# Performance work log

Hardware: AMD Instinct MI355X
Metric: run time of the kernel (lower is better)

## Reference

```python
import jax, jax.numpy as jnp
import numpy as np

EPS = 1e-12  # torch F.normalize eps


def setup_inputs() -> dict:
    key = jax.random.key(0)
    k1, k2, k3 = jax.random.split(key, 3)
    B, way, shot, D, H, W = 64, 5, 1, 640, 5, 5
    nq = 75
    base = jax.random.normal(k1, (B, way, shot, D, H, W), dtype=jnp.float32)
    query = jax.random.normal(k2, (B, nq, D, H, W), dtype=jnp.float32)
    r = jax.random.normal(k3, (2,), dtype=jnp.float32) * 0.1
    return {"base": base, "query": query, "r": r, "neighbor_k": 5}


def reference(base, query, r, neighbor_k):
    B, way, shot, D, H, W = base.shape
    nq = query.shape[1]
    hw = H * W

    # ---- global-cosine branch: spatial-mean descriptors ----
    base_mean = base.reshape(B, way * shot, D, hw).mean(axis=-1)   # [B, way*shot, D]
    query_mean = query.reshape(B, nq, D, hw).mean(axis=-1)         # [B, nq, D]
    bm = base_mean / jnp.maximum(jnp.linalg.norm(base_mean, axis=-1, keepdims=True), EPS)
    qm = query_mean / jnp.maximum(jnp.linalg.norm(query_mean, axis=-1, keepdims=True), EPS)
    logits = jnp.einsum('bqd,bkd->bqk', qm, bm)                    # [B, nq, way*shot]

    # ---- DN4 image-to-class branch (vectorized over the original triple loop) ----
    # query local descriptors: [B, nq, hw, D], L2-normalized over channels
    q = query.reshape(B, nq, D, hw).transpose(0, 1, 3, 2)
    q = q / jnp.linalg.norm(q, axis=-1, keepdims=True)
    # support local descriptors: base_mix [B, way, shot*D, hw], column-normalized
    s = base.reshape(B, way, shot * D, hw)
    s = s / jnp.linalg.norm(s, axis=2, keepdims=True)
    # cosine sims between every query patch and every support patch of each class
    # (requires shot*D == D, i.e. shot == 1, as in the original code)
    sim = jnp.einsum('bqpd,bkdl->bqkpl', q, s)                     # [B, nq, way, hw, hw]
    topk_vals, _ = jax.lax.top_k(sim, neighbor_k)                  # [B, nq, way, hw, k]
    logits_dn4 = topk_vals.sum(axis=(-1, -2)) / neighbor_k         # [B, nq, way]

    return r[0] * logits + r[1] * logits_dn4
```

## Files before the change

### kernel.cpp

```cpp
#include <hip/hip_runtime.h>
#include <hip/hip_bf16.h>
#include <math.h>

#define NB    64
#define WAY   5
#define DCH   640
#define HW    25
#define NQ    75
#define NBK   5
#define EPSN  1e-12f

#define QPB   4
#define BPB   ((NQ + QPB - 1) / QPB)
#define NDG   (DCH / 8)
#define SCOLS 128

typedef __attribute__((ext_vector_type(8)))  short  bf16x8;
typedef __attribute__((ext_vector_type(8)))  ushort u16x8;
typedef __attribute__((ext_vector_type(16))) float  f32x16;
typedef __attribute__((ext_vector_type(4)))  float  f32x4;

__device__ inline ushort f2bf(float f) {
    uint u = __float_as_uint(f);
    return (ushort)((u + 0x7FFFu + ((u >> 16) & 1u)) >> 16);
}

__global__ __launch_bounds__(256) void k_prep(const float* __restrict__ base,
                                              float* __restrict__ invs,
                                              float* __restrict__ invsm,
                                              ushort* __restrict__ sT)
{
    const int bk = blockIdx.x;
    const int b  = bk / WAY;
    const int k  = bk - b * WAY;
    const float* src = base + (size_t)bk * (DCH * HW);
    __shared__ float lds[DCH * HW];
    __shared__ float red[256];
    const int tid = threadIdx.x;

    const f32x4* s4 = (const f32x4*)src;
    f32x4* l4 = (f32x4*)lds;
    for (int i = tid; i < (DCH * HW) / 4; i += 256)
        l4[i] = __builtin_nontemporal_load(s4 + i);
    __syncthreads();

    if (tid < HW) {
        float ss = 0.f;
        for (int d = 0; d < DCH; ++d) { float v = lds[d * HW + tid]; ss = fmaf(v, v, ss); }
        invs[bk * HW + tid] = rsqrtf(ss);
    }

    float ssq = 0.f;
    for (int d = tid; d < DCH; d += 256) {
        float s = 0.f;
        #pragma unroll
        for (int pp = 0; pp < HW; ++pp) s += lds[d * HW + pp];
        float m = s * (1.0f / HW);
        ssq = fmaf(m, m, ssq);
    }
    red[tid] = ssq;
    __syncthreads();
    for (int s = 128; s > 0; s >>= 1) {
        if (tid < s) red[tid] += red[tid + s];
        __syncthreads();
    }
    if (tid == 0) invsm[bk] = 1.0f / fmaxf(sqrtf(red[0]), EPSN);

    ushort* dstb = sT + (size_t)b * (NDG * SCOLS * 8);
    for (int t = tid; t < NDG * HW; t += 256) {
        const int dg = t / HW, l = t - dg * HW;
        u16x8 v;
        #pragma unroll
        for (int e = 0; e < 8; ++e) v[e] = f2bf(lds[(dg * 8 + e) * HW + l]);
        *(u16x8*)&dstb[((size_t)dg * SCOLS + k * HW + l) * 8] = v;
    }
    if (k == 0) {
        const u16x8 z = (u16x8)(ushort)0;
        for (int t = tid; t < NDG * 3; t += 256) {
            const int dg = t / 3, sc = 125 + (t - dg * 3);
            *(u16x8*)&dstb[((size_t)dg * SCOLS + sc) * 8] = z;
        }
    }
}

__global__ __launch_bounds__(256, 3) void k_fused(const float* __restrict__ query,
                                                  const ushort* __restrict__ sT,
                                                  const float* __restrict__ invs,
                                                  const float* __restrict__ invsm,
                                                  const float* __restrict__ r,
                                                  float* __restrict__ out)
{
    __shared__ float invs_l[WAY * HW];
    __shared__ float invsm_l[WAY];

    const int tid  = threadIdx.x;
    const int wid  = tid >> 6;
    const int lane = tid & 63;
    const int p    = lane & 31;
    const int hi   = lane >> 5;

    const int wk = (blockIdx.x & 7) * (int)(gridDim.x >> 3) + (blockIdx.x >> 3);
    const int b  = wk / BPB;
    const int qb = wk - b * BPB;
    const int q  = qb * QPB + wid;
    const bool qok = q < NQ;

    if (tid < WAY * HW) invs_l[tid] = invs[b * WAY * HW + tid];
    if (tid < WAY)      invsm_l[tid] = invsm[b * WAY + tid];
    __syncthreads();
    if (!qok) return;

    f32x16 acc0 = {}, acc1 = {}, acc2 = {}, acc3 = {}, accg = {};
    float ssq = 0.f;

    const int pc = (p < HW) ? p : (HW - 1);
    const float* qp = query + (size_t)(b * NQ + q) * (DCH * HW) + pc;
    const ushort* sTb = sT + (size_t)b * (NDG * SCOLS * 8);

    #pragma unroll 4
    for (int st = 0; st < DCH / 16; ++st) {
        const int dg = st * 2 + hi;
        const float* qs = qp + (size_t)(st * 16 + hi * 8) * HW;
        bf16x8 bq;
        #pragma unroll
        for (int e = 0; e < 8; ++e) {
            const float v = __builtin_nontemporal_load(qs + e * HW);
            ssq = fmaf(v, v, ssq);
            bq[e] = (short)f2bf(v);
        }
        const bf16x8* arow = (const bf16x8*)(sTb + (size_t)dg * SCOLS * 8);
        const bf16x8 a0 = arow[p];
        const bf16x8 a1 = arow[32 + p];
        const bf16x8 a2 = arow[64 + p];
        const bf16x8 a3 = arow[96 + p];
        acc0 = __builtin_amdgcn_mfma_f32_32x32x16_bf16(a0, bq, acc0, 0, 0, 0);
        acc1 = __builtin_amdgcn_mfma_f32_32x32x16_bf16(a1, bq, acc1, 0, 0, 0);
        acc2 = __builtin_amdgcn_mfma_f32_32x32x16_bf16(a2, bq, acc2, 0, 0, 0);
        acc3 = __builtin_amdgcn_mfma_f32_32x32x16_bf16(a3, bq, acc3, 0, 0, 0);
        accg = __builtin_amdgcn_mfma_f32_32x32x16_bf16(bq, bq, accg, 0, 0, 0);
    }

    const bool pok = p < HW;

    ssq += __shfl_xor(ssq, 32);
    const float invq = rsqrtf(ssq);

    float gs[WAY] = {0.f, 0.f, 0.f, 0.f, 0.f};
    float qq = 0.f;
    #pragma unroll
    for (int rr = 0; rr < 16; ++rr) {
        const int rowb = (rr & 3) + 8 * (rr >> 2);
        const float v0 = hi ? 0.f : accg[rr];
        const float v1 = hi ? accg[rr] : 0.f;
        if (rowb < HW)     qq += v0;
        if (rowb + 4 < HW) qq += v1;
    }
#define TILE_SUM(ACC, T)                                            \
    _Pragma("unroll")                                               \
    for (int rr = 0; rr < 16; ++rr) {                               \
        const int s0 = (T) * 32 + (rr & 3) + 8 * (rr >> 2);         \
        const float v0 = hi ? 0.f : ACC[rr];                        \
        const float v1 = hi ? ACC[rr] : 0.f;                        \
        if (s0 < 125)     gs[s0 / 25]       += v0;                  \
        if (s0 + 4 < 125) gs[(s0 + 4) / 25] += v1;                  \
    }
    TILE_SUM(acc0, 0) TILE_SUM(acc1, 1) TILE_SUM(acc2, 2) TILE_SUM(acc3, 3)
#undef TILE_SUM

    if (!pok) {
        qq = 0.f;
        #pragma unroll
        for (int g = 0; g < WAY; ++g) gs[g] = 0.f;
    }
    #pragma unroll
    for (int o = 1; o < 64; o <<= 1) {
        qq += __shfl_xor(qq, o);
        #pragma unroll
        for (int g = 0; g < WAY; ++g) gs[g] += __shfl_xor(gs[g], o);
    }

    float A[64];
    #pragma unroll
    for (int rr = 0; rr < 16; ++rr) {
        A[rr] = acc0[rr]; A[16 + rr] = acc1[rr]; A[32 + rr] = acc2[rr]; A[48 + rr] = acc3[rr];
    }

    float tots[WAY];
    #pragma unroll
    for (int g = 0; g < WAY; ++g) {
        float v[HW];
        #pragma unroll
        for (int j = 0; j < HW; ++j) {
            const int scol = g * HW + j;
            const int t = scol >> 5, row = scol & 31;
            const int hreq = (row >> 2) & 1;
            const int rr = (row & 3) | ((row >> 3) << 2);
            float mine = (hi == hreq) ? A[t * 16 + rr] : 0.f;
            mine += __shfl_xor(mine, 32);
            v[j] = mine * invq * invs_l[scol];
        }
        float gtot = 0.f;
        #pragma unroll
        for (int it = 0; it < NBK; ++it) {
            float m = v[0];
            #pragma unroll
            for (int j = 1; j < HW; ++j) m = fmaxf(m, v[j]);
            gtot += m;
            bool rem = false;
            #pragma unroll
            for (int j = 0; j < HW; ++j) {
                const bool hit = (!rem) && (v[j] == m);
                v[j] = hit ? -3.402823466e38f : v[j];
                rem = rem || hit;
            }
        }
        tots[g] = pok ? gtot : 0.f;
    }
    #pragma unroll
    for (int o = 1; o < 64; o <<= 1) {
        #pragma unroll
        for (int g = 0; g < WAY; ++g) tots[g] += __shfl_xor(tots[g], o);
    }

    const float r0 = r[0], r1 = r[1];
    const float invqm = 1.0f / fmaxf(sqrtf(qq) * (1.0f / HW), EPSN);
    float res[WAY];
    #pragma unroll
    for (int g = 0; g < WAY; ++g)
        res[g] = r0 * gs[g] * (1.0f / 625.0f) * invqm * invsm_l[g]
               + r1 * tots[g] * 0.5f * (1.0f / NBK);

    float ov = res[0];
    ov = (lane == 1) ? res[1] : ov;
    ov = (lane == 2) ? res[2] : ov;
    ov = (lane == 3) ? res[3] : ov;
    ov = (lane == 4) ? res[4] : ov;
    if (lane < WAY) out[(size_t)(b * NQ + q) * WAY + lane] = ov;
}

extern "C" void kernel_launch(void* const* d_in, const int* in_sizes, int n_in,
                              void* d_out, int out_size, void* d_ws, size_t ws_size,
                              hipStream_t stream)
{
    const float* base  = (const float*)d_in[0];
    const float* query = (const float*)d_in[1];
    const float* r     = (const float*)d_in[2];
    float* out = (float*)d_out;

    float* invs   = (float*)d_ws;
    float* invsm  = invs + NB * WAY * HW;
    ushort* sT    = (ushort*)((float*)d_ws + 16384);

    k_prep<<<NB * WAY, 256, 0, stream>>>(base, invs, invsm, sT);
    k_fused<<<NB * BPB, 256, 0, stream>>>(query, sT, invs, invsm, r, out);
}
```

Before: 134.2 us.

## Stage query chunks through double-buffered LDS with coalesced vector loads

Replaces the strided per-element nontemporal global loads of the query (stride HW floats per lane) with coalesced float4 loads of contiguous 64-channel chunks into a per-wave double-buffered LDS region. The next chunk is loaded into registers while MFMAs run on the current one, then written to LDS. The aim is to cut uncoalesced global traffic and hide load latency. It adds about 51 KB of LDS per block, which may reduce occupancy below the launch-bounds target of 3 blocks, and it relies on per-wave buffers without explicit barriers.

```diff
diff --git a/kernel.cpp b/kernel.cpp
--- a/kernel.cpp
+++ b/kernel.cpp
@@ -14,6 +14,9 @@
 #define BPB   ((NQ + QPB - 1) / QPB)
 #define NDG   (DCH / 8)
 #define SCOLS 128
+#define CD    64
+#define NCHK  (DCH / CD)
+#define CFL   (CD * HW)
 
 typedef __attribute__((ext_vector_type(8)))  short  bf16x8;
 typedef __attribute__((ext_vector_type(8)))  ushort u16x8;
@@ -90,6 +93,7 @@
                                                   const float* __restrict__ r,
                                                   float* __restrict__ out)
 {
+    __shared__ __align__(16) float lds_q[QPB][2][CFL];
     __shared__ float invs_l[WAY * HW];
     __shared__ float invsm_l[WAY];
 
@@ -114,31 +118,63 @@
     float ssq = 0.f;
 
     const int pc = (p < HW) ? p : (HW - 1);
-    const float* qp = query + (size_t)(b * NQ + q) * (DCH * HW) + pc;
+    const float* qrow = query + (size_t)(b * NQ + q) * (DCH * HW);
     const ushort* sTb = sT + (size_t)b * (NDG * SCOLS * 8);
 
-    #pragma unroll 4
-    for (int st = 0; st < DCH / 16; ++st) {
-        const int dg = st * 2 + hi;
-        const float* qs = qp + (size_t)(st * 16 + hi * 8) * HW;
-        bf16x8 bq;
-        #pragma unroll
-        for (int e = 0; e < 8; ++e) {
-            const float v = __builtin_nontemporal_load(qs + e * HW);
-            ssq = fmaf(v, v, ssq);
-            bq[e] = (short)f2bf(v);
-        }
-        const bf16x8* arow = (const bf16x8*)(sTb + (size_t)dg * SCOLS * 8);
-        const bf16x8 a0 = arow[p];
-        const bf16x8 a1 = arow[32 + p];
-        const bf16x8 a2 = arow[64 + p];
-        const bf16x8 a3 = arow[96 + p];
-        acc0 = __builtin_amdgcn_mfma_f32_32x32x16_bf16(a0, bq, acc0, 0, 0, 0);
-        acc1 = __builtin_amdgcn_mfma_f32_32x32x16_bf16(a1, bq, acc1, 0, 0, 0);
-        acc2 = __builtin_amdgcn_mfma_f32_32x32x16_bf16(a2, bq, acc2, 0, 0, 0);
-        acc3 = __builtin_amdgcn_mfma_f32_32x32x16_bf16(a3, bq, acc3, 0, 0, 0);
-        accg = __builtin_amdgcn_mfma_f32_32x32x16_bf16(bq, bq, accg, 0, 0, 0);
-    }
+    f32x4 ld[7];
+
+#define LOADC(c)                                                              \
+    {                                                                         \
+        const float* src_ = qrow + (c) * CFL;                                 \
+        _Pragma("unroll")                                                     \
+        for (int i = 0; i < 6; ++i)                                           \
+            ld[i] = __builtin_nontemporal_load((const f32x4*)(src_) + i * 64 + lane); \
+        if (lane < 16)                                                        \
+            ld[6] = __builtin_nontemporal_load((const f32x4*)(src_) + 384 + lane); \
+    }
+
+#define WRITEC(buf)                                                           \
+    {                                                                         \
+        f32x4* dst_ = (f32x4*)&lds_q[wid][(buf)][0];                          \
+        _Pragma("unroll")                                                     \
+        for (int i = 0; i < 6; ++i) dst_[i * 64 + lane] = ld[i];              \
+        if (lane < 16) dst_[384 + lane] = ld[6];                              \
+    }
+
+    LOADC(0)
+    WRITEC(0)
+
+    for (int c = 0; c < NCHK; ++c) {
+        const int cur = c & 1;
+        if (c + 1 < NCHK) LOADC(c + 1)
+
+        const float* qb_lds = &lds_q[wid][cur][hi * 8 * HW + pc];
+        #pragma unroll
+        for (int ks = 0; ks < CD / 16; ++ks) {
+            const int dg = c * 8 + ks * 2 + hi;
+            bf16x8 bq;
+            #pragma unroll
+            for (int e = 0; e < 8; ++e) {
+                const float v = qb_lds[(ks * 16 + e) * HW];
+                ssq = fmaf(v, v, ssq);
+                bq[e] = (short)f2bf(v);
+            }
+            const bf16x8* arow = (const bf16x8*)(sTb + (size_t)dg * SCOLS * 8);
+            const bf16x8 a0 = arow[p];
+            const bf16x8 a1 = arow[32 + p];
+            const bf16x8 a2 = arow[64 + p];
+            const bf16x8 a3 = arow[96 + p];
+            acc0 = __builtin_amdgcn_mfma_f32_32x32x16_bf16(a0, bq, acc0, 0, 0, 0);
+            acc1 = __builtin_amdgcn_mfma_f32_32x32x16_bf16(a1, bq, acc1, 0, 0, 0);
+            acc2 = __builtin_amdgcn_mfma_f32_32x32x16_bf16(a2, bq, acc2, 0, 0, 0);
+            acc3 = __builtin_amdgcn_mfma_f32_32x32x16_bf16(a3, bq, acc3, 0, 0, 0);
+            accg = __builtin_amdgcn_mfma_f32_32x32x16_bf16(bq, bq, accg, 0, 0, 0);
+        }
+
+        if (c + 1 < NCHK) WRITEC((c + 1) & 1)
+    }
+#undef LOADC
+#undef WRITEC
 
     const bool pok = p < HW;
 
```

After: 130.5 us. -2.7%, faster.

## Stage query chunks through LDS with async double-buffered loads and streaming top-k

Applied to the files above, without the earlier changes.

Replaces strided per-lane global loads of the query with asynchronous global_load_lds copies of contiguous 64-channel chunks into a per-wave double buffer in LDS. The next chunk's copy is overlapped with the MFMA work on the current one. The epilogue now pre-scales the accumulators by the support norms and replaces the repeated max-and-remove top-5 with a streaming 5-slot insertion network, dropping the 64-float staging array. This adds about 50 KB of LDS per block, which may reduce occupancy, and it depends on hand-placed waitcnt ordering being correct.

```diff
diff --git a/kernel.cpp b/kernel.cpp
--- a/kernel.cpp
+++ b/kernel.cpp
@@ -14,6 +14,9 @@
 #define BPB   ((NQ + QPB - 1) / QPB)
 #define NDG   (DCH / 8)
 #define SCOLS 128
+#define CD    64
+#define NCHK  (DCH / CD)
+#define CFL   (CD * HW)
 
 typedef __attribute__((ext_vector_type(8)))  short  bf16x8;
 typedef __attribute__((ext_vector_type(8)))  ushort u16x8;
@@ -90,7 +93,8 @@
                                                   const float* __restrict__ r,
                                                   float* __restrict__ out)
 {
-    __shared__ float invs_l[WAY * HW];
+    __shared__ __align__(16) float lds_q[QPB][2][CFL];
+    __shared__ float invs_l[SCOLS];
     __shared__ float invsm_l[WAY];
 
     const int tid  = threadIdx.x;
@@ -106,6 +110,7 @@
     const bool qok = q < NQ;
 
     if (tid < WAY * HW) invs_l[tid] = invs[b * WAY * HW + tid];
+    if (tid >= WAY * HW && tid < SCOLS) invs_l[tid] = 0.f;
     if (tid < WAY)      invsm_l[tid] = invsm[b * WAY + tid];
     __syncthreads();
     if (!qok) return;
@@ -114,31 +119,60 @@
     float ssq = 0.f;
 
     const int pc = (p < HW) ? p : (HW - 1);
-    const float* qp = query + (size_t)(b * NQ + q) * (DCH * HW) + pc;
+    const float* qrow = query + (size_t)(b * NQ + q) * (DCH * HW);
     const ushort* sTb = sT + (size_t)b * (NDG * SCOLS * 8);
 
-    #pragma unroll 4
-    for (int st = 0; st < DCH / 16; ++st) {
-        const int dg = st * 2 + hi;
-        const float* qs = qp + (size_t)(st * 16 + hi * 8) * HW;
-        bf16x8 bq;
-        #pragma unroll
-        for (int e = 0; e < 8; ++e) {
-            const float v = __builtin_nontemporal_load(qs + e * HW);
-            ssq = fmaf(v, v, ssq);
-            bq[e] = (short)f2bf(v);
-        }
-        const bf16x8* arow = (const bf16x8*)(sTb + (size_t)dg * SCOLS * 8);
-        const bf16x8 a0 = arow[p];
-        const bf16x8 a1 = arow[32 + p];
-        const bf16x8 a2 = arow[64 + p];
-        const bf16x8 a3 = arow[96 + p];
-        acc0 = __builtin_amdgcn_mfma_f32_32x32x16_bf16(a0, bq, acc0, 0, 0, 0);
-        acc1 = __builtin_amdgcn_mfma_f32_32x32x16_bf16(a1, bq, acc1, 0, 0, 0);
-        acc2 = __builtin_amdgcn_mfma_f32_32x32x16_bf16(a2, bq, acc2, 0, 0, 0);
-        acc3 = __builtin_amdgcn_mfma_f32_32x32x16_bf16(a3, bq, acc3, 0, 0, 0);
-        accg = __builtin_amdgcn_mfma_f32_32x32x16_bf16(bq, bq, accg, 0, 0, 0);
-    }
+#define ISSUE(c)                                                               \
+    {                                                                          \
+        const float* src_ = qrow + (c) * CFL;                                  \
+        float* dst_ = &lds_q[wid][(c) & 1][0];                                 \
+        _Pragma("unroll")                                                      \
+        for (int i = 0; i < 6; ++i)                                            \
+            __builtin_amdgcn_global_load_lds(                                  \
+                (const __attribute__((address_space(1))) uint*)(src_ + i * 256 + lane * 4), \
+                (__attribute__((address_space(3))) uint*)(dst_ + i * 256), 16, 0, 0); \
+        if (lane < 16)                                                         \
+            __builtin_amdgcn_global_load_lds(                                  \
+                (const __attribute__((address_space(1))) uint*)(src_ + 1536 + lane * 4), \
+                (__attribute__((address_space(3))) uint*)(dst_ + 1536), 16, 0, 0); \
+    }
+
+    ISSUE(0)
+
+    for (int c = 0; c < NCHK; ++c) {
+        if (c + 1 < NCHK) {
+            asm volatile("s_waitcnt lgkmcnt(0)" ::: "memory");
+            ISSUE(c + 1)
+            asm volatile("s_waitcnt vmcnt(7)" ::: "memory");
+        } else {
+            asm volatile("s_waitcnt vmcnt(0)" ::: "memory");
+        }
+        __builtin_amdgcn_sched_barrier(0);
+
+        const float* qb_lds = &lds_q[wid][c & 1][hi * 8 * HW + pc];
+        #pragma unroll
+        for (int ks = 0; ks < CD / 16; ++ks) {
+            const int dg = c * 8 + ks * 2 + hi;
+            bf16x8 bq;
+            #pragma unroll
+            for (int e = 0; e < 8; ++e) {
+                const float v = qb_lds[(ks * 16 + e) * HW];
+                ssq = fmaf(v, v, ssq);
+                bq[e] = (short)f2bf(v);
+            }
+            const bf16x8* arow = (const bf16x8*)(sTb + (size_t)dg * SCOLS * 8);
+            const bf16x8 a0 = arow[p];
+            const bf16x8 a1 = arow[32 + p];
+            const bf16x8 a2 = arow[64 + p];
+            const bf16x8 a3 = arow[96 + p];
+            acc0 = __builtin_amdgcn_mfma_f32_32x32x16_bf16(a0, bq, acc0, 0, 0, 0);
+            acc1 = __builtin_amdgcn_mfma_f32_32x32x16_bf16(a1, bq, acc1, 0, 0, 0);
+            acc2 = __builtin_amdgcn_mfma_f32_32x32x16_bf16(a2, bq, acc2, 0, 0, 0);
+            acc3 = __builtin_amdgcn_mfma_f32_32x32x16_bf16(a3, bq, acc3, 0, 0, 0);
+            accg = __builtin_amdgcn_mfma_f32_32x32x16_bf16(bq, bq, accg, 0, 0, 0);
+        }
+    }
+#undef ISSUE
 
     const bool pok = p < HW;
 
@@ -179,42 +213,37 @@
         for (int g = 0; g < WAY; ++g) gs[g] += __shfl_xor(gs[g], o);
     }
 
-    float A[64];
-    #pragma unroll
-    for (int rr = 0; rr < 16; ++rr) {
-        A[rr] = acc0[rr]; A[16 + rr] = acc1[rr]; A[32 + rr] = acc2[rr]; A[48 + rr] = acc3[rr];
-    }
+#define SCALE(ACC, T)                                               \
+    _Pragma("unroll")                                               \
+    for (int rr = 0; rr < 16; ++rr) {                               \
+        const int s0 = (T) * 32 + (rr & 3) + 8 * (rr >> 2);         \
+        ACC[rr] *= invs_l[s0 + 4 * hi];                             \
+    }
+    SCALE(acc0, 0) SCALE(acc1, 1) SCALE(acc2, 2) SCALE(acc3, 3)
+#undef SCALE
 
     float tots[WAY];
     #pragma unroll
     for (int g = 0; g < WAY; ++g) {
-        float v[HW];
+        float t0 = -3.402823466e38f, t1 = t0, t2 = t0, t3 = t0, t4 = t0;
         #pragma unroll
         for (int j = 0; j < HW; ++j) {
             const int scol = g * HW + j;
             const int t = scol >> 5, row = scol & 31;
             const int hreq = (row >> 2) & 1;
             const int rr = (row & 3) | ((row >> 3) << 2);
-            float mine = (hi == hreq) ? A[t * 16 + rr] : 0.f;
+            const float av = (t == 0) ? acc0[rr] : (t == 1) ? acc1[rr]
+                           : (t == 2) ? acc2[rr] : acc3[rr];
+            float mine = (hi == hreq) ? av : 0.f;
             mine += __shfl_xor(mine, 32);
-            v[j] = mine * invq * invs_l[scol];
-        }
-        float gtot = 0.f;
-        #pragma unroll
-        for (int it = 0; it < NBK; ++it) {
-            float m = v[0];
-            #pragma unroll
-            for (int j = 1; j < HW; ++j) m = fmaxf(m, v[j]);
-            gtot += m;
-            bool rem = false;
-            #pragma unroll
-            for (int j = 0; j < HW; ++j) {
-                const bool hit = (!rem) && (v[j] == m);
-                v[j] = hit ? -3.402823466e38f : v[j];
-                rem = rem || hit;
-            }
-        }
-        tots[g] = pok ? gtot : 0.f;
+            float x = mine, a;
+            a = fmaxf(t0, x); x = fminf(t0, x); t0 = a;
+            a = fmaxf(t1, x); x = fminf(t1, x); t1 = a;
+            a = fmaxf(t2, x); x = fminf(t2, x); t2 = a;
+            a = fmaxf(t3, x); x = fminf(t3, x); t3 = a;
+            a = fmaxf(t4, x); x = fminf(t4, x); t4 = a;
+        }
+        tots[g] = pok ? (t0 + t1 + t2 + t3 + t4) * invq : 0.f;
     }
     #pragma unroll
     for (int o = 1; o < 64; o <<= 1) {
```

New measurement: 117.4 us. -12.5%, faster.

## Restructure fused kernel to one query per block with coalesced LDS-staged loads

Applied to the files above, without the earlier changes.

Each block now handles a single query image, and its four waves each compute one 32-column tile of support columns. Query data is loaded with coalesced float4 nontemporal loads into a double-buffered LDS staging area in bf16 MFMA layout, replacing per-lane strided scalar loads. The per-patch query norm now comes from the diagonal of the bf16 Gram MFMA instead of an fp32 sum of squares, which slightly changes precision. Top-k runs as a five-slot insertion network over LDS-transposed similarities, and more barriers are added in exchange for better load coalescing and occupancy.

```diff
diff --git a/kernel.cpp b/kernel.cpp
--- a/kernel.cpp
+++ b/kernel.cpp
@@ -10,10 +10,13 @@
 #define NBK   5
 #define EPSN  1e-12f
 
-#define QPB   4
-#define BPB   ((NQ + QPB - 1) / QPB)
 #define NDG   (DCH / 8)
 #define SCOLS 128
+#define CD    160
+#define NCHK  (DCH / CD)
+#define DGC   (CD / 8)
+#define CFL   (CD * HW)
+#define CTS   132
 
 typedef __attribute__((ext_vector_type(8)))  short  bf16x8;
 typedef __attribute__((ext_vector_type(8)))  ushort u16x8;
@@ -83,14 +86,15 @@
     }
 }
 
-__global__ __launch_bounds__(256, 3) void k_fused(const float* __restrict__ query,
+__global__ __launch_bounds__(256, 4) void k_fused(const float* __restrict__ query,
                                                   const ushort* __restrict__ sT,
                                                   const float* __restrict__ invs,
                                                   const float* __restrict__ invsm,
                                                   const float* __restrict__ r,
                                                   float* __restrict__ out)
 {
-    __shared__ float invs_l[WAY * HW];
+    __shared__ ushort s_bq[2][DGC * 32 * 8];
+    __shared__ float invs_l[SCOLS];
     __shared__ float invsm_l[WAY];
 
     const int tid  = threadIdx.x;
@@ -99,143 +103,170 @@
     const int p    = lane & 31;
     const int hi   = lane >> 5;
 
-    const int wk = (blockIdx.x & 7) * (int)(gridDim.x >> 3) + (blockIdx.x >> 3);
-    const int b  = wk / BPB;
-    const int qb = wk - b * BPB;
-    const int q  = qb * QPB + wid;
-    const bool qok = q < NQ;
+    const int wk = (blockIdx.x & 7) * 600 + (blockIdx.x >> 3);
+    const int b  = wk / NQ;
+    const int q  = wk - b * NQ;
 
     if (tid < WAY * HW) invs_l[tid] = invs[b * WAY * HW + tid];
+    if (tid >= WAY * HW && tid < SCOLS) invs_l[tid] = 0.f;
     if (tid < WAY)      invsm_l[tid] = invsm[b * WAY + tid];
-    __syncthreads();
-    if (!qok) return;
-
-    f32x16 acc0 = {}, acc1 = {}, acc2 = {}, acc3 = {}, accg = {};
-    float ssq = 0.f;
-
-    const int pc = (p < HW) ? p : (HW - 1);
-    const float* qp = query + (size_t)(b * NQ + q) * (DCH * HW) + pc;
+
+    const float* qrow = query + (size_t)(b * NQ + q) * (DCH * HW);
     const ushort* sTb = sT + (size_t)b * (NDG * SCOLS * 8);
 
-    #pragma unroll 4
-    for (int st = 0; st < DCH / 16; ++st) {
-        const int dg = st * 2 + hi;
-        const float* qs = qp + (size_t)(st * 16 + hi * 8) * HW;
-        bf16x8 bq;
-        #pragma unroll
-        for (int e = 0; e < 8; ++e) {
-            const float v = __builtin_nontemporal_load(qs + e * HW);
-            ssq = fmaf(v, v, ssq);
-            bq[e] = (short)f2bf(v);
-        }
-        const bf16x8* arow = (const bf16x8*)(sTb + (size_t)dg * SCOLS * 8);
-        const bf16x8 a0 = arow[p];
-        const bf16x8 a1 = arow[32 + p];
-        const bf16x8 a2 = arow[64 + p];
-        const bf16x8 a3 = arow[96 + p];
-        acc0 = __builtin_amdgcn_mfma_f32_32x32x16_bf16(a0, bq, acc0, 0, 0, 0);
-        acc1 = __builtin_amdgcn_mfma_f32_32x32x16_bf16(a1, bq, acc1, 0, 0, 0);
-        acc2 = __builtin_amdgcn_mfma_f32_32x32x16_bf16(a2, bq, acc2, 0, 0, 0);
-        acc3 = __builtin_amdgcn_mfma_f32_32x32x16_bf16(a3, bq, acc3, 0, 0, 0);
-        accg = __builtin_amdgcn_mfma_f32_32x32x16_bf16(bq, bq, accg, 0, 0, 0);
-    }
+    f32x16 accT = {}, accG = {};
+    f32x4 lA0 = {}, lA1 = {}, lA2 = {}, lA3 = {};
+    f32x4 lB0 = {}, lB1 = {}, lB2 = {}, lB3 = {};
+
+#define LOADQ(c, R0, R1, R2, R3)                                              \
+    {                                                                         \
+        const f32x4* s4_ = (const f32x4*)(qrow + (size_t)(c) * CFL);          \
+        R0 = __builtin_nontemporal_load(s4_ + tid);                           \
+        R1 = __builtin_nontemporal_load(s4_ + 256 + tid);                     \
+        R2 = __builtin_nontemporal_load(s4_ + 512 + tid);                     \
+        if (tid < 232) R3 = __builtin_nontemporal_load(s4_ + 768 + tid);      \
+    }
+
+#define WR4(DST, SLOT, V)                                                     \
+    {                                                                         \
+        _Pragma("unroll")                                                     \
+        for (int j = 0; j < 4; ++j) {                                         \
+            const int flat = (SLOT) * 4 + j;                                  \
+            const int d  = flat / 25;                                         \
+            const int pp = flat - d * 25;                                     \
+            (DST)[((d >> 3) * 32 + pp) * 8 + (d & 7)] = f2bf((V)[j]);         \
+        }                                                                     \
+    }
+
+#define WRITEQ(BUF, R0, R1, R2, R3)                                           \
+    {                                                                         \
+        ushort* db_ = &s_bq[BUF][0];                                          \
+        WR4(db_, tid, R0)                                                     \
+        WR4(db_, 256 + tid, R1)                                               \
+        WR4(db_, 512 + tid, R2)                                               \
+        if (tid < 232) WR4(db_, 768 + tid, R3)                                \
+    }
+
+#define COMPUTE(BUF, C)                                                       \
+    {                                                                         \
+        _Pragma("unroll")                                                     \
+        for (int ks = 0; ks < DGC / 2; ++ks) {                                \
+            const int dgl = ks * 2 + hi;                                      \
+            const bf16x8 bq = *(const bf16x8*)&s_bq[BUF][(dgl * 32 + p) * 8]; \
+            const bf16x8 a  = *(const bf16x8*)(sTb +                          \
+                ((size_t)((C) * DGC + dgl) * SCOLS + wid * 32 + p) * 8);      \
+            accT = __builtin_amdgcn_mfma_f32_32x32x16_bf16(a,  bq, accT, 0, 0, 0); \
+            accG = __builtin_amdgcn_mfma_f32_32x32x16_bf16(bq, bq, accG, 0, 0, 0); \
+        }                                                                     \
+    }
+
+    LOADQ(0, lA0, lA1, lA2, lA3)
+    for (int i = tid; i < 2 * DGC * 7; i += 256) {
+        const int bu = i / (DGC * 7), r2 = i % (DGC * 7);
+        const int dg = r2 / 7, s = r2 % 7;
+        *(u16x8*)&s_bq[bu][((dg * 32) + 25 + s) * 8] = (u16x8)(ushort)0;
+    }
+    WRITEQ(0, lA0, lA1, lA2, lA3)
+    __syncthreads();
+    LOADQ(1, lB0, lB1, lB2, lB3)
+    COMPUTE(0, 0)
+    __syncthreads();
+    LOADQ(2, lA0, lA1, lA2, lA3)
+    WRITEQ(1, lB0, lB1, lB2, lB3)
+    __syncthreads();
+    COMPUTE(1, 1)
+    __syncthreads();
+    LOADQ(3, lB0, lB1, lB2, lB3)
+    WRITEQ(0, lA0, lA1, lA2, lA3)
+    __syncthreads();
+    COMPUTE(0, 2)
+    __syncthreads();
+    WRITEQ(1, lB0, lB1, lB2, lB3)
+    __syncthreads();
+    COMPUTE(1, 3)
+
+#undef LOADQ
+#undef WR4
+#undef WRITEQ
+#undef COMPUTE
 
     const bool pok = p < HW;
 
-    ssq += __shfl_xor(ssq, 32);
-    const float invq = rsqrtf(ssq);
-
-    float gs[WAY] = {0.f, 0.f, 0.f, 0.f, 0.f};
-    float qq = 0.f;
+    float diag = 0.f, qq = 0.f;
     #pragma unroll
     for (int rr = 0; rr < 16; ++rr) {
         const int rowb = (rr & 3) + 8 * (rr >> 2);
-        const float v0 = hi ? 0.f : accg[rr];
-        const float v1 = hi ? accg[rr] : 0.f;
-        if (rowb < HW)     qq += v0;
-        if (rowb + 4 < HW) qq += v1;
-    }
-#define TILE_SUM(ACC, T)                                            \
-    _Pragma("unroll")                                               \
-    for (int rr = 0; rr < 16; ++rr) {                               \
-        const int s0 = (T) * 32 + (rr & 3) + 8 * (rr >> 2);         \
-        const float v0 = hi ? 0.f : ACC[rr];                        \
-        const float v1 = hi ? ACC[rr] : 0.f;                        \
-        if (s0 < 125)     gs[s0 / 25]       += v0;                  \
-        if (s0 + 4 < 125) gs[(s0 + 4) / 25] += v1;                  \
-    }
-    TILE_SUM(acc0, 0) TILE_SUM(acc1, 1) TILE_SUM(acc2, 2) TILE_SUM(acc3, 3)
-#undef TILE_SUM
-
-    if (!pok) {
-        qq = 0.f;
-        #pragma unroll
-        for (int g = 0; g < WAY; ++g) gs[g] = 0.f;
-    }
+        const int row = rowb + 4 * hi;
+        diag = (row == p) ? accG[rr] : diag;
+        if (row < HW) qq += accG[rr];
+    }
+    if (!pok) qq = 0.f;
     #pragma unroll
-    for (int o = 1; o < 64; o <<= 1) {
-        qq += __shfl_xor(qq, o);
-        #pragma unroll
-        for (int g = 0; g < WAY; ++g) gs[g] += __shfl_xor(gs[g], o);
-    }
-
-    float A[64];
+    for (int o = 1; o < 64; o <<= 1) qq += __shfl_xor(qq, o);
+    diag += __shfl_xor(diag, 32);
+    const float invq = rsqrtf(diag);
+
+    float cs16[16];
     #pragma unroll
     for (int rr = 0; rr < 16; ++rr) {
-        A[rr] = acc0[rr]; A[16 + rr] = acc1[rr]; A[32 + rr] = acc2[rr]; A[48 + rr] = acc3[rr];
-    }
-
-    float tots[WAY];
-    #pragma unroll
-    for (int g = 0; g < WAY; ++g) {
-        float v[HW];
+        float tv = pok ? accT[rr] : 0.f;
+        #pragma unroll
+        for (int o = 1; o < 32; o <<= 1) tv += __shfl_xor(tv, o);
+        cs16[rr] = tv;
+    }
+
+    __syncthreads();
+
+    float* ct       = (float*)&s_bq[0][0];
+    float* cs_lds   = ct + HW * CTS;
+    float* tops_lds = cs_lds + SCOLS;
+
+    if (p == 0) {
+        #pragma unroll
+        for (int rr = 0; rr < 16; ++rr) {
+            const int rowb = (rr & 3) + 8 * (rr >> 2);
+            cs_lds[wid * 32 + rowb + 4 * hi] = cs16[rr];
+        }
+    }
+    if (pok) {
+        #pragma unroll
+        for (int rr = 0; rr < 16; ++rr) {
+            const int rowb = (rr & 3) + 8 * (rr >> 2);
+            const int scol = wid * 32 + rowb + 4 * hi;
+            ct[p * CTS + scol] = accT[rr] * invq * invs_l[scol];
+        }
+    }
+    __syncthreads();
+
+    if (tid < WAY * HW) {
+        const int way = tid / HW, pp = tid - way * HW;
+        const float* row = &ct[pp * CTS + way * HW];
+        float t0 = -3.402823466e38f, t1 = t0, t2 = t0, t3 = t0, t4 = t0;
         #pragma unroll
         for (int j = 0; j < HW; ++j) {
-            const int scol = g * HW + j;
-            const int t = scol >> 5, row = scol & 31;
-            const int hreq = (row >> 2) & 1;
-            const int rr = (row & 3) | ((row >> 3) << 2);
-            float mine = (hi == hreq) ? A[t * 16 + rr] : 0.f;
-            mine += __shfl_xor(mine, 32);
-            v[j] = mine * invq * invs_l[scol];
-        }
-        float gtot = 0.f;
-        #pragma unroll
-        for (int it = 0; it < NBK; ++it) {
-            float m = v[0];
-            #pragma unroll
-            for (int j = 1; j < HW; ++j) m = fmaxf(m, v[j]);
-            gtot += m;
-            bool rem = false;
-            #pragma unroll
-            for (int j = 0; j < HW; ++j) {
-                const bool hit = (!rem) && (v[j] == m);
-                v[j] = hit ? -3.402823466e38f : v[j];
-                rem = rem || hit;
-            }
-        }
-        tots[g] = pok ? gtot : 0.f;
-    }
-    #pragma unroll
-    for (int o = 1; o < 64; o <<= 1) {
-        #pragma unroll
-        for (int g = 0; g < WAY; ++g) tots[g] += __shfl_xor(tots[g], o);
-    }
-
-    const float r0 = r[0], r1 = r[1];
-    const float invqm = 1.0f / fmaxf(sqrtf(qq) * (1.0f / HW), EPSN);
-    float res[WAY];
-    #pragma unroll
-    for (int g = 0; g < WAY; ++g)
-        res[g] = r0 * gs[g] * (1.0f / 625.0f) * invqm * invsm_l[g]
-               + r1 * tots[g] * 0.5f * (1.0f / NBK);
-
-    float ov = res[0];
-    ov = (lane == 1) ? res[1] : ov;
-    ov = (lane == 2) ? res[2] : ov;
-    ov = (lane == 3) ? res[3] : ov;
-    ov = (lane == 4) ? res[4] : ov;
-    if (lane < WAY) out[(size_t)(b * NQ + q) * WAY + lane] = ov;
+            float x = row[j], a;
+            a = fmaxf(t0, x); x = fminf(t0, x); t0 = a;
+            a = fmaxf(t1, x); x = fminf(t1, x); t1 = a;
+            a = fmaxf(t2, x); x = fminf(t2, x); t2 = a;
+            a = fmaxf(t3, x); x = fminf(t3, x); t3 = a;
+            a = fmaxf(t4, x); x = fminf(t4, x); t4 = a;
+        }
+        tops_lds[tid] = t0 + t1 + t2 + t3 + t4;
+    }
+    __syncthreads();
+
+    if (tid < WAY) {
+        float gsv = 0.f, dn = 0.f;
+        #pragma unroll
+        for (int j = 0; j < HW; ++j) {
+            gsv += cs_lds[tid * HW + j];
+            dn  += tops_lds[tid * HW + j];
+        }
+        const float invqm = 1.0f / fmaxf(sqrtf(qq) * (1.0f / HW), EPSN);
+        out[(size_t)(b * NQ + q) * WAY + tid] =
+            r[0] * gsv * (1.0f / 625.0f) * invqm * invsm_l[tid]
+          + r[1] * dn * (1.0f / NBK);
+    }
 }
 
 extern "C" void kernel_launch(void* const* d_in, const int* in_sizes, int n_in,
@@ -252,5 +283,5 @@
     ushort* sT    = (ushort*)((float*)d_ws + 16384);
 
     k_prep<<<NB * WAY, 256, 0, stream>>>(base, invs, invsm, sT);
-    k_fused<<<NB * BPB, 256, 0, stream>>>(query, sT, invs, invsm, r, out);
-}
+    k_fused<<<NB * NQ, 256, 0, stream>>>(query, sT, invs, invsm, r, out);
+}
```

Measured after the change: 119.0 us. 11.3% less time.
